# Kernel tuning notes

Hardware: AMD Instinct MI355X
Metric: run time of the kernel (lower is better)

The kernel has to match this reference:

```python
import jax, jax.numpy as jnp
import numpy as np

SHRINK_THRES = 0.0025
R_THRES = 1.0
EPS = 1e-12


def setup_inputs() -> dict:
    key = jax.random.key(0)
    k1, k2 = jax.random.split(key)
    N, L, D = 16384, 4096, 1024  # samples, memory slots (lan_dim), fea_dim
    x = jax.random.normal(k1, (N, D), dtype=jnp.float32)
    stdv = 1.0 / np.sqrt(D)
    weight = jax.random.uniform(k2, (L, D), dtype=jnp.float32, minval=-stdv, maxval=stdv)
    return {"x": x, "weight": weight}


def reference(x, weight):
    # memory addressing: att = softmax(x @ W^T)  -> [N, L]
    att = jax.nn.softmax(x @ weight.T, axis=1)
    # hard_shrink_relu: relu(a - lambd) * a / (|a - lambd| + eps)
    shifted = att - SHRINK_THRES
    att = jax.nn.relu(shifted) * att / (jnp.abs(shifted) + EPS)
    # L1 normalize along dim 1 (F.normalize p=1, eps=1e-12)
    l1 = jnp.sum(jnp.abs(att), axis=1, keepdims=True)
    att = att / jnp.maximum(l1, EPS)
    # reconstruct from memory: [N, D]
    output = att @ weight
    # nearest landmark per sample (detached gather in original)
    ind = jnp.argmax(att, axis=1)                      # [N]
    nl = weight[ind]                                   # [N, D]
    # second-nearest: overwrite argmax slot with the row minimum, re-argmax
    rows = jnp.arange(att.shape[0])
    row_min = jnp.min(att, axis=1)
    att2 = att.at[rows, ind].set(row_min)
    ind2 = jnp.argmax(att2, axis=1)
    nl2 = weight[ind2]                                 # [N, D]
    # centroid-distance filter (original returns list of indices; we return a
    # jit-compatible boolean mask over samples instead)
    cen = jnp.mean(weight, axis=0)                     # [D]
    dist = jnp.sqrt(jnp.sum((x - cen) ** 2, axis=1))   # [N]
    col_mask = dist < R_THRES                          # [N] bool
    return (output, att, nl, nl2, col_mask)
```

## Files before the change

kernel.cpp:

```cpp
#include <hip/hip_runtime.h>
#include <cmath>

#define NS 16384
#define LS 4096
#define DF 1024
#define SHRINK_T 0.0025f
#define EPS_T 1e-12f

using f16 = _Float16;
using f16x4 = __attribute__((ext_vector_type(4))) _Float16;
using f16x8 = __attribute__((ext_vector_type(8))) _Float16;
using f32x4 = __attribute__((ext_vector_type(4))) float;

#define NSEG 64

__global__ void split_kernel(const float* __restrict__ src,
                             f16* __restrict__ hi, f16* __restrict__ lo, int n4) {
    int i = blockIdx.x * 256 + threadIdx.x;
    if (i >= n4) return;
    float4 v = reinterpret_cast<const float4*>(src)[i];
    f16x4 h, l;
    h[0] = (f16)v.x; h[1] = (f16)v.y; h[2] = (f16)v.z; h[3] = (f16)v.w;
    l[0] = (f16)(v.x - (float)h[0]);
    l[1] = (f16)(v.y - (float)h[1]);
    l[2] = (f16)(v.z - (float)h[2]);
    l[3] = (f16)(v.w - (float)h[3]);
    reinterpret_cast<f16x4*>(hi)[i] = h;
    reinterpret_cast<f16x4*>(lo)[i] = l;
}

__global__ void centroid_part_kernel(const float* __restrict__ w, float* __restrict__ part) {
    const int c = blockIdx.x * 256 + threadIdx.x;
    const int seg = blockIdx.y;
    const int l0 = seg * (LS / NSEG);
    float acc = 0.f;
    for (int l = 0; l < LS / NSEG; ++l)
        acc += w[(size_t)(l0 + l) * DF + c];
    part[(size_t)seg * DF + c] = acc;
}

__global__ void centroid_sum_kernel(const float* __restrict__ part, float* __restrict__ cen) {
    const int c = blockIdx.x * 256 + threadIdx.x;
    float acc = 0.f;
    for (int s = 0; s < NSEG; ++s) acc += part[(size_t)s * DF + c];
    cen[c] = acc * (1.0f / (float)LS);
}

#define BM 128
#define BN 128
#define BK 32

#define GLOAD16(gptr, lptr)                                                    \
    __builtin_amdgcn_global_load_lds(                                          \
        (const __attribute__((address_space(1))) void*)(gptr),                 \
        (__attribute__((address_space(3))) void*)(lptr), 16, 0, 0)

__device__ __forceinline__ int swz_s(int r) { return (r & 3) ^ ((r >> 2) & 1); }

__global__ __launch_bounds__(256, 2) void gemm_f16_kernel(
    const f16* __restrict__ xh, const f16* __restrict__ xl,
    const f16* __restrict__ wh, const f16* __restrict__ wl,
    float* __restrict__ S, int r0, int rowsChunk)
{
    __shared__ __align__(16) f16 Ah[2][BM * BK];
    __shared__ __align__(16) f16 Al[2][BM * BK];
    __shared__ __align__(16) f16 Bh[2][BN * BK];
    __shared__ __align__(16) f16 Bl[2][BN * BK];

    const int t = threadIdx.x;
    const int lane = t & 63;
    const int wv = t >> 6;
    const int wr = (wv >> 1) * 64;
    const int wc = (wv & 1) * 64;
    const int rowBase = r0 + blockIdx.y * BM;
    const int colBase = blockIdx.x * BN;

    f32x4 acc[4][4];
#pragma unroll
    for (int m = 0; m < 4; ++m)
#pragma unroll
        for (int n = 0; n < 4; ++n)
            acc[m][n] = (f32x4){0.f, 0.f, 0.f, 0.f};

    const int fr = lane & 15;
    const int fq = lane >> 4;

    const int sr_lo = t >> 2;
    const int cc_lo = ((t & 3) ^ swz_s(sr_lo)) * 8;
    const int sr_hi = 64 + sr_lo;
    const int cc_hi = ((t & 3) ^ swz_s(sr_hi)) * 8;
    int ga_lo = rowBase + sr_lo; if (ga_lo >= NS) ga_lo = NS - 1;
    int ga_hi = rowBase + sr_hi; if (ga_hi >= NS) ga_hi = NS - 1;
    const size_t aoff_lo = (size_t)ga_lo * DF + cc_lo;
    const size_t aoff_hi = (size_t)ga_hi * DF + cc_hi;
    const size_t boff_lo = (size_t)(colBase + sr_lo) * DF + cc_lo;
    const size_t boff_hi = (size_t)(colBase + sr_hi) * DF + cc_hi;
    const int lb_lo = (wv * 16) * BK;
    const int lb_hi = (64 + wv * 16) * BK;

#define STAGE(k0, b)                                         \
    do {                                                     \
        GLOAD16(xh + aoff_lo + (k0), &Ah[b][lb_lo]);         \
        GLOAD16(xl + aoff_lo + (k0), &Al[b][lb_lo]);         \
        GLOAD16(wh + boff_lo + (k0), &Bh[b][lb_lo]);         \
        GLOAD16(wl + boff_lo + (k0), &Bl[b][lb_lo]);         \
        GLOAD16(xh + aoff_hi + (k0), &Ah[b][lb_hi]);         \
        GLOAD16(xl + aoff_hi + (k0), &Al[b][lb_hi]);         \
        GLOAD16(wh + boff_hi + (k0), &Bh[b][lb_hi]);         \
        GLOAD16(wl + boff_hi + (k0), &Bl[b][lb_hi]);         \
    } while (0)

    STAGE(0, 0);

    for (int kt = 0; kt < DF / BK; ++kt) {
        const int b = kt & 1;
        __syncthreads();
        if (kt + 1 < DF / BK) STAGE((kt + 1) * BK, b ^ 1);

        f16x8 amh[4], aml[4], bnh[4], bnl[4];
#pragma unroll
        for (int m = 0; m < 4; ++m) {
            const int r = wr + m * 16 + fr;
            const int ca = (fq ^ swz_s(r)) * 8;
            amh[m] = *(const f16x8*)&Ah[b][r * BK + ca];
            aml[m] = *(const f16x8*)&Al[b][r * BK + ca];
        }
#pragma unroll
        for (int n = 0; n < 4; ++n) {
            const int c = wc + n * 16 + fr;
            const int cb = (fq ^ swz_s(c)) * 8;
            bnh[n] = *(const f16x8*)&Bh[b][c * BK + cb];
            bnl[n] = *(const f16x8*)&Bl[b][c * BK + cb];
        }
        __builtin_amdgcn_s_setprio(1);
#pragma unroll
        for (int m = 0; m < 4; ++m)
#pragma unroll
            for (int n = 0; n < 4; ++n) {
                acc[m][n] = __builtin_amdgcn_mfma_f32_16x16x32_f16(amh[m], bnh[n], acc[m][n], 0, 0, 0);
                acc[m][n] = __builtin_amdgcn_mfma_f32_16x16x32_f16(amh[m], bnl[n], acc[m][n], 0, 0, 0);
                acc[m][n] = __builtin_amdgcn_mfma_f32_16x16x32_f16(aml[m], bnh[n], acc[m][n], 0, 0, 0);
            }
        __builtin_amdgcn_s_setprio(0);
    }
#undef STAGE

#pragma unroll
    for (int m = 0; m < 4; ++m) {
        const int rbase = blockIdx.y * BM + wr + m * 16 + fq * 4;
#pragma unroll
        for (int n = 0; n < 4; ++n) {
            const int cc = colBase + wc + n * 16 + fr;
#pragma unroll
            for (int j = 0; j < 4; ++j) {
                const int rr = rbase + j;
                if (rr < rowsChunk)
                    S[(size_t)rr * LS + cc] = acc[m][n][j];
            }
        }
    }
}

__global__ __launch_bounds__(256) void pass2_kernel(
    const float* __restrict__ S, const float* __restrict__ x,
    const float* __restrict__ w, const float* __restrict__ cen,
    float* __restrict__ out, int r0)
{
    constexpr int T = 256;
    __shared__ __align__(16) float att_lds[LS];
    __shared__ float red[T];
    __shared__ int redi[T];

    const int t = threadIdx.x;
    const size_t row = (size_t)r0 + blockIdx.x;
    const float4* s4 = (const float4*)(S + (size_t)blockIdx.x * (size_t)LS);

    float* const out_output = out;
    float* const out_att  = out + (size_t)NS * DF;
    float* const out_nl   = out + (size_t)NS * DF + (size_t)NS * LS;
    float* const out_nl2  = out + (size_t)2 * NS * DF + (size_t)NS * LS;
    float* const out_mask = out + (size_t)3 * NS * DF + (size_t)NS * LS;

    float sv[16];
    float mx = -INFINITY;
#pragma unroll
    for (int i = 0; i < 4; ++i) {
        float4 v = s4[i * 256 + t];
        sv[i * 4 + 0] = v.x; sv[i * 4 + 1] = v.y;
        sv[i * 4 + 2] = v.z; sv[i * 4 + 3] = v.w;
        mx = fmaxf(mx, fmaxf(fmaxf(v.x, v.y), fmaxf(v.z, v.w)));
    }
    red[t] = mx;
    __syncthreads();
    for (int off = 128; off >= 1; off >>= 1) {
        if (t < off) red[t] = fmaxf(red[t], red[t + off]);
        __syncthreads();
    }
    const float m = red[0];
    __syncthreads();

    float zs = 0.f;
#pragma unroll
    for (int i = 0; i < 16; ++i) {
        sv[i] = expf(sv[i] - m);
        zs += sv[i];
    }
    red[t] = zs;
    __syncthreads();
    for (int off = 128; off >= 1; off >>= 1) {
        if (t < off) red[t] += red[t + off];
        __syncthreads();
    }
    const float Z = red[0];
    __syncthreads();

    float l1 = 0.f;
#pragma unroll
    for (int i = 0; i < 16; ++i) {
        float a = sv[i] / Z;
        float r = a - SHRINK_T;
        float v = (r > 0.f) ? (r * a) / (r + EPS_T) : 0.f;
        sv[i] = v;
        l1 += v;
    }
    red[t] = l1;
    __syncthreads();
    for (int off = 128; off >= 1; off >>= 1) {
        if (t < off) red[t] += red[t + off];
        __syncthreads();
    }
    const float nrm = fmaxf(red[0], EPS_T);
    __syncthreads();

    float bv = -INFINITY; int bi = LS;
    float mn = INFINITY;
    float4* const attl4 = (float4*)att_lds;
    float4* const att4o = (float4*)(out_att + row * LS);
#pragma unroll
    for (int i = 0; i < 4; ++i) {
        float4 vn4;
        vn4.x = sv[i * 4 + 0] / nrm; vn4.y = sv[i * 4 + 1] / nrm;
        vn4.z = sv[i * 4 + 2] / nrm; vn4.w = sv[i * 4 + 3] / nrm;
        sv[i * 4 + 0] = vn4.x; sv[i * 4 + 1] = vn4.y;
        sv[i * 4 + 2] = vn4.z; sv[i * 4 + 3] = vn4.w;
        attl4[i * 256 + t] = vn4;
        att4o[i * 256 + t] = vn4;
#pragma unroll
        for (int c = 0; c < 4; ++c) {
            const float v = sv[i * 4 + c];
            const int j = i * 1024 + 4 * t + c;
            if (v > bv) { bv = v; bi = j; }
            mn = fminf(mn, v);
        }
    }
    __syncthreads();

    red[t] = bv; redi[t] = bi;
    __syncthreads();
    for (int off = 128; off >= 1; off >>= 1) {
        if (t < off) {
            float ov = red[t + off]; int oi = redi[t + off];
            if (ov > red[t] || (ov == red[t] && oi < redi[t])) { red[t] = ov; redi[t] = oi; }
        }
        __syncthreads();
    }
    const int ind = redi[0];
    __syncthreads();

    red[t] = mn;
    __syncthreads();
    for (int off = 128; off >= 1; off >>= 1) {
        if (t < off) red[t] = fminf(red[t], red[t + off]);
        __syncthreads();
    }
    const float rowmin = red[0];
    __syncthreads();

    bv = -INFINITY; bi = LS;
#pragma unroll
    for (int i = 0; i < 4; ++i)
#pragma unroll
        for (int c = 0; c < 4; ++c) {
            const int j = i * 1024 + 4 * t + c;
            const float vv = (j == ind) ? rowmin : sv[i * 4 + c];
            if (vv > bv) { bv = vv; bi = j; }
        }
    red[t] = bv; redi[t] = bi;
    __syncthreads();
    for (int off = 128; off >= 1; off >>= 1) {
        if (t < off) {
            float ov = red[t + off]; int oi = redi[t + off];
            if (ov > red[t] || (ov == red[t] && oi < redi[t])) { red[t] = ov; redi[t] = oi; }
        }
        __syncthreads();
    }
    const int ind2 = redi[0];
    __syncthreads();

    const int lane = t & 63;
    float4 oa = {0.f, 0.f, 0.f, 0.f};
    for (int k0 = 0; k0 < LS; k0 += 64) {
        float av = att_lds[k0 + lane];
        unsigned long long msk = __ballot(av > 0.f);
        while (msk) {
            int b = __ffsll((unsigned long long)msk) - 1;
            msk &= msk - 1;
            float vv = att_lds[k0 + b];
            float4 wv4 = ((const float4*)(w + (size_t)(k0 + b) * DF))[t];
            oa.x = fmaf(vv, wv4.x, oa.x);
            oa.y = fmaf(vv, wv4.y, oa.y);
            oa.z = fmaf(vv, wv4.z, oa.z);
            oa.w = fmaf(vv, wv4.w, oa.w);
        }
    }
    ((float4*)(out_output + row * DF))[t] = oa;

    ((float4*)(out_nl  + row * DF))[t] = ((const float4*)(w + (size_t)ind  * DF))[t];
    ((float4*)(out_nl2 + row * DF))[t] = ((const float4*)(w + (size_t)ind2 * DF))[t];

    float4 xv = ((const float4*)(x + row * DF))[t];
    float4 cv = ((const float4*)cen)[t];
    float ds = 0.f;
    ds = fmaf(xv.x - cv.x, xv.x - cv.x, ds);
    ds = fmaf(xv.y - cv.y, xv.y - cv.y, ds);
    ds = fmaf(xv.z - cv.z, xv.z - cv.z, ds);
    ds = fmaf(xv.w - cv.w, xv.w - cv.w, ds);
    red[t] = ds;
    __syncthreads();
    for (int off = 128; off >= 1; off >>= 1) {
        if (t < off) red[t] += red[t + off];
        __syncthreads();
    }
    if (t == 0) {
        float dist = sqrtf(red[0]);
        out_mask[row] = (dist < 1.0f) ? 1.0f : 0.0f;
    }
}

extern "C" void kernel_launch(void* const* d_in, const int* in_sizes, int n_in,
                              void* d_out, int out_size, void* d_ws, size_t ws_size,
                              hipStream_t stream)
{
    const float* x = (const float*)d_in[0];
    const float* w = (const float*)d_in[1];
    float* out = (float*)d_out;

    float* cen = (float*)d_ws;
    float* part = cen + DF;
    f16* xh = (f16*)(part + (size_t)NSEG * DF);
    f16* xl = xh + (size_t)NS * DF;
    f16* wh = xl + (size_t)NS * DF;
    f16* wl = wh + (size_t)LS * DF;
    float* S = (float*)(wl + (size_t)LS * DF);

    const size_t head_bytes = sizeof(float) * (DF + (size_t)NSEG * DF)
                            + (size_t)2 * 2 * NS * DF + (size_t)2 * 2 * LS * DF;
    long cap_rows = (long)((ws_size - head_bytes) / (sizeof(float) * LS));
    if (cap_rows > NS) cap_rows = NS;
    if (cap_rows < 1) cap_rows = 1;
    int chunk = (cap_rows >= BM) ? (int)(cap_rows - (cap_rows % BM)) : (int)cap_rows;

    centroid_part_kernel<<<dim3(DF / 256, NSEG), 256, 0, stream>>>(w, part);
    centroid_sum_kernel<<<DF / 256, 256, 0, stream>>>(part, cen);
    split_kernel<<<(NS * DF / 4 + 255) / 256, 256, 0, stream>>>(x, xh, xl, NS * DF / 4);
    split_kernel<<<(LS * DF / 4 + 255) / 256, 256, 0, stream>>>(w, wh, wl, LS * DF / 4);

    for (int r0 = 0; r0 < NS; r0 += chunk) {
        int rows = (NS - r0 < chunk) ? (NS - r0) : chunk;
        dim3 grid((LS + BN - 1) / BN, (rows + BM - 1) / BM);
        gemm_f16_kernel<<<grid, 256, 0, stream>>>(xh, xl, wh, wl, S, r0, rows);
        pass2_kernel<<<rows, 256, 0, stream>>>(S, x, w, cen, out, r0);
    }
}
```

Baseline: 598.7 us.

## Switch GEMM to 32x32x16 MFMA tiles and drop LDS double buffering

```diff
diff --git a/kernel.cpp b/kernel.cpp
--- a/kernel.cpp
+++ b/kernel.cpp
@@ -10,7 +10,7 @@
 using f16 = _Float16;
 using f16x4 = __attribute__((ext_vector_type(4))) _Float16;
 using f16x8 = __attribute__((ext_vector_type(8))) _Float16;
-using f32x4 = __attribute__((ext_vector_type(4))) float;
+using f32x16 = __attribute__((ext_vector_type(16))) float;
 
 #define NSEG 64
 
@@ -57,15 +57,15 @@
 
 __device__ __forceinline__ int swz_s(int r) { return (r & 3) ^ ((r >> 2) & 1); }
 
-__global__ __launch_bounds__(256, 2) void gemm_f16_kernel(
+__global__ __launch_bounds__(256) void gemm_f16_kernel(
     const f16* __restrict__ xh, const f16* __restrict__ xl,
     const f16* __restrict__ wh, const f16* __restrict__ wl,
     float* __restrict__ S, int r0, int rowsChunk)
 {
-    __shared__ __align__(16) f16 Ah[2][BM * BK];
-    __shared__ __align__(16) f16 Al[2][BM * BK];
-    __shared__ __align__(16) f16 Bh[2][BN * BK];
-    __shared__ __align__(16) f16 Bl[2][BN * BK];
+    __shared__ __align__(16) f16 Ah[BM * BK];
+    __shared__ __align__(16) f16 Al[BM * BK];
+    __shared__ __align__(16) f16 Bh[BN * BK];
+    __shared__ __align__(16) f16 Bl[BN * BK];
 
     const int t = threadIdx.x;
     const int lane = t & 63;
@@ -75,15 +75,16 @@
     const int rowBase = r0 + blockIdx.y * BM;
     const int colBase = blockIdx.x * BN;
 
-    f32x4 acc[4][4];
-#pragma unroll
-    for (int m = 0; m < 4; ++m)
-#pragma unroll
-        for (int n = 0; n < 4; ++n)
-            acc[m][n] = (f32x4){0.f, 0.f, 0.f, 0.f};
-
-    const int fr = lane & 15;
-    const int fq = lane >> 4;
+    f32x16 acc[2][2];
+#pragma unroll
+    for (int m = 0; m < 2; ++m)
+#pragma unroll
+        for (int n = 0; n < 2; ++n)
+#pragma unroll
+            for (int j = 0; j < 16; ++j) acc[m][n][j] = 0.f;
+
+    const int c32 = lane & 31;
+    const int kh = lane >> 5;
 
     const int sr_lo = t >> 2;
     const int cc_lo = ((t & 3) ^ swz_s(sr_lo)) * 8;
@@ -98,64 +99,57 @@
     const int lb_lo = (wv * 16) * BK;
     const int lb_hi = (64 + wv * 16) * BK;
 
-#define STAGE(k0, b)                                         \
-    do {                                                     \
-        GLOAD16(xh + aoff_lo + (k0), &Ah[b][lb_lo]);         \
-        GLOAD16(xl + aoff_lo + (k0), &Al[b][lb_lo]);         \
-        GLOAD16(wh + boff_lo + (k0), &Bh[b][lb_lo]);         \
-        GLOAD16(wl + boff_lo + (k0), &Bl[b][lb_lo]);         \
-        GLOAD16(xh + aoff_hi + (k0), &Ah[b][lb_hi]);         \
-        GLOAD16(xl + aoff_hi + (k0), &Al[b][lb_hi]);         \
-        GLOAD16(wh + boff_hi + (k0), &Bh[b][lb_hi]);         \
-        GLOAD16(wl + boff_hi + (k0), &Bl[b][lb_hi]);         \
-    } while (0)
-
-    STAGE(0, 0);
-
-    for (int kt = 0; kt < DF / BK; ++kt) {
-        const int b = kt & 1;
-        __syncthreads();
-        if (kt + 1 < DF / BK) STAGE((kt + 1) * BK, b ^ 1);
-
-        f16x8 amh[4], aml[4], bnh[4], bnl[4];
-#pragma unroll
-        for (int m = 0; m < 4; ++m) {
-            const int r = wr + m * 16 + fr;
-            const int ca = (fq ^ swz_s(r)) * 8;
-            amh[m] = *(const f16x8*)&Ah[b][r * BK + ca];
-            aml[m] = *(const f16x8*)&Al[b][r * BK + ca];
-        }
-#pragma unroll
-        for (int n = 0; n < 4; ++n) {
-            const int c = wc + n * 16 + fr;
-            const int cb = (fq ^ swz_s(c)) * 8;
-            bnh[n] = *(const f16x8*)&Bh[b][c * BK + cb];
-            bnl[n] = *(const f16x8*)&Bl[b][c * BK + cb];
-        }
-        __builtin_amdgcn_s_setprio(1);
-#pragma unroll
-        for (int m = 0; m < 4; ++m)
-#pragma unroll
-            for (int n = 0; n < 4; ++n) {
-                acc[m][n] = __builtin_amdgcn_mfma_f32_16x16x32_f16(amh[m], bnh[n], acc[m][n], 0, 0, 0);
-                acc[m][n] = __builtin_amdgcn_mfma_f32_16x16x32_f16(amh[m], bnl[n], acc[m][n], 0, 0, 0);
-                acc[m][n] = __builtin_amdgcn_mfma_f32_16x16x32_f16(aml[m], bnh[n], acc[m][n], 0, 0, 0);
+    for (int k0 = 0; k0 < DF; k0 += BK) {
+        GLOAD16(xh + aoff_lo + k0, &Ah[lb_lo]);
+        GLOAD16(xl + aoff_lo + k0, &Al[lb_lo]);
+        GLOAD16(wh + boff_lo + k0, &Bh[lb_lo]);
+        GLOAD16(wl + boff_lo + k0, &Bl[lb_lo]);
+        GLOAD16(xh + aoff_hi + k0, &Ah[lb_hi]);
+        GLOAD16(xl + aoff_hi + k0, &Al[lb_hi]);
+        GLOAD16(wh + boff_hi + k0, &Bh[lb_hi]);
+        GLOAD16(wl + boff_hi + k0, &Bl[lb_hi]);
+        __syncthreads();
+
+#pragma unroll
+        for (int s = 0; s < 2; ++s) {
+            f16x8 amh[2], aml[2], bnh[2], bnl[2];
+#pragma unroll
+            for (int m = 0; m < 2; ++m) {
+                const int r = wr + m * 32 + c32;
+                const int q = ((s * 2 + kh) ^ swz_s(r)) * 8;
+                amh[m] = *(const f16x8*)&Ah[r * BK + q];
+                aml[m] = *(const f16x8*)&Al[r * BK + q];
             }
-        __builtin_amdgcn_s_setprio(0);
-    }
-#undef STAGE
-
-#pragma unroll
-    for (int m = 0; m < 4; ++m) {
-        const int rbase = blockIdx.y * BM + wr + m * 16 + fq * 4;
-#pragma unroll
-        for (int n = 0; n < 4; ++n) {
-            const int cc = colBase + wc + n * 16 + fr;
-#pragma unroll
-            for (int j = 0; j < 4; ++j) {
-                const int rr = rbase + j;
+#pragma unroll
+            for (int n = 0; n < 2; ++n) {
+                const int c = wc + n * 32 + c32;
+                const int q = ((s * 2 + kh) ^ swz_s(c)) * 8;
+                bnh[n] = *(const f16x8*)&Bh[c * BK + q];
+                bnl[n] = *(const f16x8*)&Bl[c * BK + q];
+            }
+#pragma unroll
+            for (int m = 0; m < 2; ++m)
+#pragma unroll
+                for (int n = 0; n < 2; ++n) {
+                    acc[m][n] = __builtin_amdgcn_mfma_f32_32x32x16_f16(amh[m], bnh[n], acc[m][n], 0, 0, 0);
+                    acc[m][n] = __builtin_amdgcn_mfma_f32_32x32x16_f16(amh[m], bnl[n], acc[m][n], 0, 0, 0);
+                    acc[m][n] = __builtin_amdgcn_mfma_f32_32x32x16_f16(aml[m], bnh[n], acc[m][n], 0, 0, 0);
+                }
+        }
+        __syncthreads();
+    }
+
+#pragma unroll
+    for (int m = 0; m < 2; ++m) {
+        const int rb = blockIdx.y * BM + wr + m * 32 + 4 * kh;
+#pragma unroll
+        for (int n = 0; n < 2; ++n) {
+            const int cc = colBase + wc + n * 32 + c32;
+#pragma unroll
+            for (int reg = 0; reg < 16; ++reg) {
+                const int rr = rb + (reg & 3) + 8 * (reg >> 2);
                 if (rr < rowsChunk)
-                    S[(size_t)rr * LS + cc] = acc[m][n][j];
+                    S[(size_t)rr * LS + cc] = acc[m][n][reg];
             }
         }
     }
```

Result: no change. 596.5 us (-0.4%).
